# Kernel tuning notes

Measured on AMD Instinct MI355X. Metric: run time of the kernel, lower is better.

The kernel has to match this reference:

```python
import jax, jax.numpy as jnp
import numpy as np

N = 8192          # total genes
B = 16            # number of ragged batch groups (equal-size here: 512 each)
D = 768           # hidden_dim
NEG = -1.0e9      # mask fill value used by the original module


def setup_inputs() -> dict:
    key = jax.random.key(0)
    ks = jax.random.split(key, 10)
    s = 0.02
    inp = {
        "gene_embeddings": jax.random.normal(ks[0], (N, D), dtype=jnp.float32),
        # sorted group ids: 16 contiguous groups of 512 genes
        "batch": (jnp.arange(N) // (N // B)).astype(jnp.int64),
        "Wq": jax.random.normal(ks[1], (D, D), dtype=jnp.float32) * s,
        "bq": jnp.zeros((D,), dtype=jnp.float32),
        "Wk": jax.random.normal(ks[2], (D, D), dtype=jnp.float32) * s,
        "bk": jnp.zeros((D,), dtype=jnp.float32),
        "Wv": jax.random.normal(ks[3], (D, D), dtype=jnp.float32) * s,
        "bv": jnp.zeros((D,), dtype=jnp.float32),
        "Wo": jax.random.normal(ks[4], (D, D), dtype=jnp.float32) * s,
        "bo": jnp.zeros((D,), dtype=jnp.float32),
        "beta": jnp.ones((1,), dtype=jnp.float32) * 0.1,
    }
    return inp


def reference(gene_embeddings, batch, Wq, bq, Wk, bk, Wv, bv, Wo, bo, beta):
    # Single-head attention over full hidden_dim (num_heads unused in original).
    x = gene_embeddings
    q = x @ Wq.T + bq                      # [N, D]
    k = x @ Wk.T + bk
    v = x @ Wv.T + bv
    scale = 1.0 / jnp.sqrt(jnp.asarray(D, dtype=x.dtype))
    scores = (q @ k.T) * scale             # [N, N]
    # block-diagonal group mask + diagonal self-mask (same -1e9 fill as torch code)
    same_group = batch[:, None] == batch[None, :]
    eye = jnp.eye(N, dtype=bool)
    allow = same_group & (~eye)
    scores = jnp.where(allow, scores, NEG)
    weights = jax.nn.softmax(scores, axis=-1)   # dropout in eval mode -> identity
    dyn = weights @ v                       # [N, D]
    dyn = dyn @ Wo.T + bo
    return x + beta * dyn
```

## Files before the change

kernel.cpp:

```cpp
#include <hip/hip_runtime.h>
#include <hip/hip_bf16.h>
#include <cstdint>

using u16 = unsigned short;
using u32 = unsigned int;

typedef __bf16 bf16x8 __attribute__((ext_vector_type(8)));
typedef float  f32x4  __attribute__((ext_vector_type(4)));

__device__ __forceinline__ u16 f2b(float f) {
    u32 u = __builtin_bit_cast(u32, f);
    u += 0x7fffu + ((u >> 16) & 1u);
    return (u16)(u >> 16);
}

__device__ __forceinline__ void gload_lds16(const u16* g, u16* l) {
    __builtin_amdgcn_global_load_lds(
        (const __attribute__((address_space(1))) void*)g,
        (__attribute__((address_space(3))) void*)l,
        16, 0, 0);
}

__launch_bounds__(256)
__global__ void pack_kernel(const float* __restrict__ x,
                            const float* __restrict__ Wq,
                            const float* __restrict__ Wk,
                            const float* __restrict__ Wv,
                            const float* __restrict__ Wo,
                            const float* __restrict__ bq,
                            const float* __restrict__ bk,
                            const float* __restrict__ bv,
                            u16* __restrict__ xb,
                            u16* __restrict__ Wqkvb,
                            u16* __restrict__ Wob,
                            float* __restrict__ bqkv)
{
    int c = blockIdx.x * 256 + threadIdx.x;
    long e = (long)c * 8;
    const float* src; u16* dst; long off;
    if (e < 6291456L)      { src = x;  dst = xb;              off = e; }
    else if (e < 6881280L) { src = Wq; dst = Wqkvb;           off = e - 6291456L; }
    else if (e < 7471104L) { src = Wk; dst = Wqkvb + 589824;  off = e - 6881280L; }
    else if (e < 8060928L) { src = Wv; dst = Wqkvb + 1179648; off = e - 7471104L; }
    else                   { src = Wo; dst = Wob;             off = e - 8060928L; }
    float4 v0 = *(const float4*)(src + off);
    float4 v1 = *(const float4*)(src + off + 4);
    union { u16 u[8]; uint4 q; } o;
    o.u[0] = f2b(v0.x); o.u[1] = f2b(v0.y); o.u[2] = f2b(v0.z); o.u[3] = f2b(v0.w);
    o.u[4] = f2b(v1.x); o.u[5] = f2b(v1.y); o.u[6] = f2b(v1.z); o.u[7] = f2b(v1.w);
    *(uint4*)(dst + off) = o.q;
    if (c < 768)        bqkv[c] = bq[c];
    else if (c < 1536)  bqkv[c] = bk[c - 768];
    else if (c < 2304)  bqkv[c] = bv[c - 1536];
}

template<int TM, int TN, int MODE>
__launch_bounds__(256)
__global__ void gemm_bt(const u16* __restrict__ A, int lda, long sAz,
                        const u16* __restrict__ B, int ldb, long sBz,
                        void* __restrict__ Cv, int ldc, long sCz,
                        int K,
                        const float* __restrict__ bias,
                        const float* __restrict__ xres,
                        const float* __restrict__ betaPtr,
                        float scale,
                        u16* __restrict__ vTout)
{
    constexpr int FI = TM / 32;
    constexpr int FJ = TN / 32;
    constexpr int CA = TM / 64;
    constexpr int CB = TN / 64;

    __shared__ u16 As[2][TM * 32];
    __shared__ u16 Bs[2][TN * 32];

    const int tid  = threadIdx.x;
    const int g    = blockIdx.z;
    const u16* Ab = A + (long)g * sAz + (long)blockIdx.y * TM * lda;
    const u16* Bb = B + (long)g * sBz + (long)blockIdx.x * TN * ldb;

    const int wave = tid >> 6, lane = tid & 63;
    const int wm = (wave >> 1) * (TM / 2), wn = (wave & 1) * (TN / 2);
    const int ln15 = lane & 15, lq = lane >> 4;

    f32x4 acc[FI][FJ];
#pragma unroll
    for (int i = 0; i < FI; i++)
#pragma unroll
        for (int j = 0; j < FJ; j++)
            acc[i][j] = (f32x4){0.f, 0.f, 0.f, 0.f};

    const int srow = lane >> 2, sc = (lane & 3) * 8;
    const u16* Ag[CA]; const u16* Bg[CB];
    int Al[CA], Bl[CB];
#pragma unroll
    for (int t = 0; t < CA; t++) {
        int c = wave * CA + t;
        Ag[t] = Ab + (long)(c * 16 + srow) * lda + sc;
        Al[t] = c * 512;
    }
#pragma unroll
    for (int t = 0; t < CB; t++) {
        int c = wave * CB + t;
        Bg[t] = Bb + (long)(c * 16 + srow) * ldb + sc;
        Bl[t] = c * 512;
    }

    const int nk = K >> 5;

#pragma unroll
    for (int t = 0; t < CA; t++) gload_lds16(Ag[t], &As[0][Al[t]]);
#pragma unroll
    for (int t = 0; t < CB; t++) gload_lds16(Bg[t], &Bs[0][Bl[t]]);

    for (int kt = 0; kt < nk; kt++) {
        const int cur = kt & 1;
        __syncthreads();
        if (kt + 1 < nk) {
            const int k0 = (kt + 1) * 32, nxt = cur ^ 1;
#pragma unroll
            for (int t = 0; t < CA; t++) gload_lds16(Ag[t] + k0, &As[nxt][Al[t]]);
#pragma unroll
            for (int t = 0; t < CB; t++) gload_lds16(Bg[t] + k0, &Bs[nxt][Bl[t]]);
        }

        bf16x8 af[FI], bfr[FJ];
#pragma unroll
        for (int i = 0; i < FI; i++)
            af[i] = *(const bf16x8*)&As[cur][(wm + i * 16 + ln15) * 32 + lq * 8];
#pragma unroll
        for (int j = 0; j < FJ; j++)
            bfr[j] = *(const bf16x8*)&Bs[cur][(wn + j * 16 + ln15) * 32 + lq * 8];
#pragma unroll
        for (int i = 0; i < FI; i++)
#pragma unroll
            for (int j = 0; j < FJ; j++)
                acc[i][j] = __builtin_amdgcn_mfma_f32_16x16x32_bf16(af[i], bfr[j], acc[i][j], 0, 0, 0);
    }

    const int baseRow = blockIdx.y * TM + wm;
    const int baseCol = blockIdx.x * TN + wn;

    if constexpr (MODE == 0) {
        if (baseCol < 1536) {
            u16* C = (u16*)Cv;
#pragma unroll
            for (int i = 0; i < FI; i++)
#pragma unroll
                for (int j = 0; j < FJ; j++)
#pragma unroll
                    for (int r = 0; r < 4; r++) {
                        int row = baseRow + i * 16 + lq * 4 + r;
                        int col = baseCol + j * 16 + ln15;
                        C[(long)row * ldc + col] = f2b(acc[i][j][r] + bias[col]);
                    }
        } else {
#pragma unroll
            for (int i = 0; i < FI; i++)
#pragma unroll
                for (int j = 0; j < FJ; j++) {
                    int col = baseCol + j * 16 + ln15;
                    float bb = bias[col];
                    ushort4 o;
                    o.x = f2b(acc[i][j][0] + bb);
                    o.y = f2b(acc[i][j][1] + bb);
                    o.z = f2b(acc[i][j][2] + bb);
                    o.w = f2b(acc[i][j][3] + bb);
                    *(ushort4*)(vTout + (long)(col - 1536) * 8192
                                + baseRow + i * 16 + lq * 4) = o;
                }
        }
    } else if constexpr (MODE == 2) {
        float* C = (float*)Cv + (long)g * sCz;
#pragma unroll
        for (int i = 0; i < FI; i++)
#pragma unroll
            for (int j = 0; j < FJ; j++)
#pragma unroll
                for (int r = 0; r < 4; r++) {
                    int row = baseRow + i * 16 + lq * 4 + r;
                    int col = baseCol + j * 16 + ln15;
                    float v = acc[i][j][r] * scale;
                    if (row == col) v = -1.0e9f;
                    C[(long)row * ldc + col] = v;
                }
    } else if constexpr (MODE == 3) {
        u16* C = (u16*)Cv + (long)g * sCz;
#pragma unroll
        for (int i = 0; i < FI; i++)
#pragma unroll
            for (int j = 0; j < FJ; j++)
#pragma unroll
                for (int r = 0; r < 4; r++) {
                    int row = baseRow + i * 16 + lq * 4 + r;
                    int col = baseCol + j * 16 + ln15;
                    C[(long)row * ldc + col] = f2b(acc[i][j][r]);
                }
    } else {
        float* C = (float*)Cv;
        float bet = betaPtr[0];
#pragma unroll
        for (int i = 0; i < FI; i++)
#pragma unroll
            for (int j = 0; j < FJ; j++)
#pragma unroll
                for (int r = 0; r < 4; r++) {
                    int row = baseRow + i * 16 + lq * 4 + r;
                    int col = baseCol + j * 16 + ln15;
                    float v = xres[(long)row * ldc + col] + bet * (acc[i][j][r] + bias[col]);
                    C[(long)row * ldc + col] = v;
                }
    }
}

__launch_bounds__(256)
__global__ void softmax_rows(const float* __restrict__ S, u16* __restrict__ P)
{
    int row  = blockIdx.x * 4 + (threadIdx.x >> 6);
    int lane = threadIdx.x & 63;
    const float* s = S + (long)row * 512 + lane * 8;
    float4 v0 = *(const float4*)s;
    float4 v1 = *(const float4*)(s + 4);
    float vv[8] = {v0.x, v0.y, v0.z, v0.w, v1.x, v1.y, v1.z, v1.w};
    float m = vv[0];
#pragma unroll
    for (int i = 1; i < 8; i++) m = fmaxf(m, vv[i]);
#pragma unroll
    for (int off = 32; off; off >>= 1) m = fmaxf(m, __shfl_xor(m, off));
    float e[8], sum = 0.f;
#pragma unroll
    for (int i = 0; i < 8; i++) { e[i] = __expf(vv[i] - m); sum += e[i]; }
#pragma unroll
    for (int off = 32; off; off >>= 1) sum += __shfl_xor(sum, off);
    float inv = 1.0f / sum;
    union { u16 u[8]; uint4 q; } o;
#pragma unroll
    for (int i = 0; i < 8; i++) o.u[i] = f2b(e[i] * inv);
    *(uint4*)(P + (long)row * 512 + lane * 8) = o.q;
}

extern "C" void kernel_launch(void* const* d_in, const int* in_sizes, int n_in,
                              void* d_out, int out_size, void* d_ws, size_t ws_size,
                              hipStream_t stream)
{
    const float* x    = (const float*)d_in[0];
    const float* Wq   = (const float*)d_in[2];
    const float* bq   = (const float*)d_in[3];
    const float* Wk   = (const float*)d_in[4];
    const float* bk   = (const float*)d_in[5];
    const float* Wv   = (const float*)d_in[6];
    const float* bv   = (const float*)d_in[7];
    const float* Wo   = (const float*)d_in[8];
    const float* bo   = (const float*)d_in[9];
    const float* beta = (const float*)d_in[10];
    float* out = (float*)d_out;

    char* ws = (char*)d_ws;
    u16*   qk    = (u16*)(ws + 0);
    u16*   dyn   = (u16*)(ws + 0);
    u16*   vT    = (u16*)(ws + 25165824);
    u16*   xb    = (u16*)(ws + 37748736);
    float* S     = (float*)(ws + 37748736);
    u16*   Wqkvb = (u16*)(ws + 50331648);
    u16*   Wob   = (u16*)(ws + 54525952);
    float* bqkv  = (float*)(ws + 55705600);
    u16*   P     = (u16*)(ws + 55714816);

    const float scale = 0.03608439182435161f;

    pack_kernel<<<4224, 256, 0, stream>>>(x, Wq, Wk, Wv, Wo, bq, bk, bv,
                                          xb, Wqkvb, Wob, bqkv);

    gemm_bt<128, 128, 0><<<dim3(18, 64, 1), 256, 0, stream>>>(
        xb, 768, 0, Wqkvb, 768, 0, (void*)qk, 1536, 0, 768,
        bqkv, nullptr, nullptr, 0.f, vT);

    gemm_bt<64, 128, 2><<<dim3(4, 8, 16), 256, 0, stream>>>(
        qk, 1536, 512L * 1536, qk + 768, 1536, 512L * 1536,
        (void*)S, 512, 512L * 512, 768, nullptr, nullptr, nullptr, scale, nullptr);

    softmax_rows<<<2048, 256, 0, stream>>>(S, P);

    gemm_bt<64, 128, 3><<<dim3(6, 8, 16), 256, 0, stream>>>(
        P, 512, 512L * 512, vT, 8192, 512L,
        (void*)dyn, 768, 512L * 768, 512, nullptr, nullptr, nullptr, 0.f, nullptr);

    gemm_bt<64, 128, 4><<<dim3(6, 128, 1), 256, 0, stream>>>(
        dyn, 768, 0, Wob, 768, 0, (void*)out, 768, 0, 768,
        bo, x, beta, 0.f, nullptr);
}
```

Baseline: 216.5 us.

## XOR-swizzle GEMM LDS tiles and use packed bf16x2 conversions

The GEMM now stores each 16x32 LDS chunk with an XOR swizzle on the 8-element column group, applied on both the global-to-LDS load offset and the fragment read offset. This is meant to cut LDS bank conflicts when waves read MFMA fragments. Separately, all fp32-to-bf16 conversions now go through a packed two-value helper that may map to a hardware pack instruction, reducing per-element integer rounding work. The swizzle also rewrites fragment addressing to assume wm and wn are multiples of 16, which holds for the tile sizes used.

After: 216.5 us. Within noise of the previous version (+0.0%).

```diff
diff --git a/kernel.cpp b/kernel.cpp
--- a/kernel.cpp
+++ b/kernel.cpp
@@ -8,6 +8,12 @@
 typedef __bf16 bf16x8 __attribute__((ext_vector_type(8)));
 typedef float  f32x4  __attribute__((ext_vector_type(4)));
 
+__device__ __forceinline__ u32 f2b2(float a, float b) {
+    __hip_bfloat162 h = __float22bfloat162_rn(float2{a, b});
+    u32 u;
+    __builtin_memcpy(&u, &h, 4);
+    return u;
+}
 __device__ __forceinline__ u16 f2b(float f) {
     u32 u = __builtin_bit_cast(u32, f);
     u += 0x7fffu + ((u >> 16) & 1u);
@@ -45,10 +51,10 @@
     else                   { src = Wo; dst = Wob;             off = e - 8060928L; }
     float4 v0 = *(const float4*)(src + off);
     float4 v1 = *(const float4*)(src + off + 4);
-    union { u16 u[8]; uint4 q; } o;
-    o.u[0] = f2b(v0.x); o.u[1] = f2b(v0.y); o.u[2] = f2b(v0.z); o.u[3] = f2b(v0.w);
-    o.u[4] = f2b(v1.x); o.u[5] = f2b(v1.y); o.u[6] = f2b(v1.z); o.u[7] = f2b(v1.w);
-    *(uint4*)(dst + off) = o.q;
+    uint4 o;
+    o.x = f2b2(v0.x, v0.y); o.y = f2b2(v0.z, v0.w);
+    o.z = f2b2(v1.x, v1.y); o.w = f2b2(v1.z, v1.w);
+    *(uint4*)(dst + off) = o;
     if (c < 768)        bqkv[c] = bq[c];
     else if (c < 1536)  bqkv[c] = bk[c - 768];
     else if (c < 2304)  bqkv[c] = bv[c - 1536];
@@ -90,7 +96,8 @@
         for (int j = 0; j < FJ; j++)
             acc[i][j] = (f32x4){0.f, 0.f, 0.f, 0.f};
 
-    const int srow = lane >> 2, sc = (lane & 3) * 8;
+    const int srow = lane >> 2;
+    const int sc   = ((lane & 3) ^ ((lane >> 4) & 3)) * 8;
     const u16* Ag[CA]; const u16* Bg[CB];
     int Al[CA], Bl[CB];
 #pragma unroll
@@ -106,6 +113,8 @@
         Bl[t] = c * 512;
     }
 
+    const int foff = ln15 * 32 + ((lq ^ (ln15 >> 2)) * 8);
+
     const int nk = K >> 5;
 
 #pragma unroll
@@ -127,10 +136,10 @@
         bf16x8 af[FI], bfr[FJ];
 #pragma unroll
         for (int i = 0; i < FI; i++)
-            af[i] = *(const bf16x8*)&As[cur][(wm + i * 16 + ln15) * 32 + lq * 8];
+            af[i] = *(const bf16x8*)&As[cur][(wm / 16 + i) * 512 + foff];
 #pragma unroll
         for (int j = 0; j < FJ; j++)
-            bfr[j] = *(const bf16x8*)&Bs[cur][(wn + j * 16 + ln15) * 32 + lq * 8];
+            bfr[j] = *(const bf16x8*)&Bs[cur][(wn / 16 + j) * 512 + foff];
 #pragma unroll
         for (int i = 0; i < FI; i++)
 #pragma unroll
@@ -147,27 +156,29 @@
 #pragma unroll
             for (int i = 0; i < FI; i++)
 #pragma unroll
-                for (int j = 0; j < FJ; j++)
-#pragma unroll
-                    for (int r = 0; r < 4; r++) {
-                        int row = baseRow + i * 16 + lq * 4 + r;
-                        int col = baseCol + j * 16 + ln15;
-                        C[(long)row * ldc + col] = f2b(acc[i][j][r] + bias[col]);
-                    }
-        } else {
-#pragma unroll
-            for (int i = 0; i < FI; i++)
-#pragma unroll
                 for (int j = 0; j < FJ; j++) {
                     int col = baseCol + j * 16 + ln15;
                     float bb = bias[col];
-                    ushort4 o;
-                    o.x = f2b(acc[i][j][0] + bb);
-                    o.y = f2b(acc[i][j][1] + bb);
-                    o.z = f2b(acc[i][j][2] + bb);
-                    o.w = f2b(acc[i][j][3] + bb);
-                    *(ushort4*)(vTout + (long)(col - 1536) * 8192
-                                + baseRow + i * 16 + lq * 4) = o;
+                    u32 p01 = f2b2(acc[i][j][0] + bb, acc[i][j][1] + bb);
+                    u32 p23 = f2b2(acc[i][j][2] + bb, acc[i][j][3] + bb);
+                    long r0 = (long)(baseRow + i * 16 + lq * 4) * ldc + col;
+                    C[r0]           = (u16)p01;
+                    C[r0 + ldc]     = (u16)(p01 >> 16);
+                    C[r0 + 2 * ldc] = (u16)p23;
+                    C[r0 + 3 * ldc] = (u16)(p23 >> 16);
+                }
+        } else {
+#pragma unroll
+            for (int i = 0; i < FI; i++)
+#pragma unroll
+                for (int j = 0; j < FJ; j++) {
+                    int col = baseCol + j * 16 + ln15;
+                    float bb = bias[col];
+                    uint2 o;
+                    o.x = f2b2(acc[i][j][0] + bb, acc[i][j][1] + bb);
+                    o.y = f2b2(acc[i][j][2] + bb, acc[i][j][3] + bb);
+                    *(uint2*)(vTout + (long)(col - 1536) * 8192
+                              + baseRow + i * 16 + lq * 4) = o;
                 }
         }
     } else if constexpr (MODE == 2) {
@@ -189,13 +200,16 @@
 #pragma unroll
         for (int i = 0; i < FI; i++)
 #pragma unroll
-            for (int j = 0; j < FJ; j++)
-#pragma unroll
-                for (int r = 0; r < 4; r++) {
-                    int row = baseRow + i * 16 + lq * 4 + r;
-                    int col = baseCol + j * 16 + ln15;
-                    C[(long)row * ldc + col] = f2b(acc[i][j][r]);
-                }
+            for (int j = 0; j < FJ; j++) {
+                int col = baseCol + j * 16 + ln15;
+                u32 p01 = f2b2(acc[i][j][0], acc[i][j][1]);
+                u32 p23 = f2b2(acc[i][j][2], acc[i][j][3]);
+                long r0 = (long)(baseRow + i * 16 + lq * 4) * ldc + col;
+                C[r0]           = (u16)p01;
+                C[r0 + ldc]     = (u16)(p01 >> 16);
+                C[r0 + 2 * ldc] = (u16)p23;
+                C[r0 + 3 * ldc] = (u16)(p23 >> 16);
+            }
     } else {
         float* C = (float*)Cv;
         float bet = betaPtr[0];
@@ -233,10 +247,12 @@
 #pragma unroll
     for (int off = 32; off; off >>= 1) sum += __shfl_xor(sum, off);
     float inv = 1.0f / sum;
-    union { u16 u[8]; uint4 q; } o;
-#pragma unroll
-    for (int i = 0; i < 8; i++) o.u[i] = f2b(e[i] * inv);
-    *(uint4*)(P + (long)row * 512 + lane * 8) = o.q;
+    uint4 o;
+    o.x = f2b2(e[0] * inv, e[1] * inv);
+    o.y = f2b2(e[2] * inv, e[3] * inv);
+    o.z = f2b2(e[4] * inv, e[5] * inv);
+    o.w = f2b2(e[6] * inv, e[7] * inv);
+    *(uint4*)(P + (long)row * 512 + lane * 8) = o;
 }
 
 extern "C" void kernel_launch(void* const* d_in, const int* in_sizes, int n_in,
```
